# Performance work log

Measured on AMD Instinct MI355X. Metric: run time of the kernel, lower is better.

Reference implementation:

```python
import jax, jax.numpy as jnp
import numpy as np

DIM = 1024
HIDDEN = 4096
NNZ = 262144
X_SHAPE = (2, 256, DIM)


def setup_inputs() -> dict:
    key = jax.random.key(0)
    ks = jax.random.split(key, 13)
    return {
        "x": jax.random.normal(ks[0], X_SHAPE, dtype=jnp.float32),
        "up_row": jax.random.randint(ks[1], (NNZ,), 0, HIDDEN),
        "up_col": jax.random.randint(ks[2], (NNZ,), 0, DIM),
        "up_val": jax.random.normal(ks[3], (NNZ,), dtype=jnp.float32),
        "up_bias": jax.random.normal(ks[4], (HIDDEN,), dtype=jnp.float32),
        "gate_row": jax.random.randint(ks[5], (NNZ,), 0, HIDDEN),
        "gate_col": jax.random.randint(ks[6], (NNZ,), 0, DIM),
        "gate_val": jax.random.normal(ks[7], (NNZ,), dtype=jnp.float32),
        "gate_bias": jax.random.normal(ks[8], (HIDDEN,), dtype=jnp.float32),
        "down_row": jax.random.randint(ks[9], (NNZ,), 0, DIM),
        "down_col": jax.random.randint(ks[10], (NNZ,), 0, HIDDEN),
        "down_val": jax.random.normal(ks[11], (NNZ,), dtype=jnp.float32),
        "down_bias": jax.random.normal(ks[12], (DIM,), dtype=jnp.float32),
    }


def _sparse_linear(x2d, row, col, val, bias, out_features):
    # x2d: [T, in_features]; COO: row -> out_features, col -> in_features
    weighted = x2d[:, col] * val  # [T, nnz], same expanded form as torch gather*mul
    # scatter_add over rows == segment_sum over the nnz axis
    out = jax.ops.segment_sum(weighted.T, row, num_segments=out_features).T  # [T, out]
    return out + bias


def reference(x, up_row, up_col, up_val, up_bias,
              gate_row, gate_col, gate_val, gate_bias,
              down_row, down_col, down_val, down_bias):
    in_shape = x.shape
    x2d = x.reshape(-1, DIM)  # [T, dim]
    up = _sparse_linear(x2d, up_row, up_col, up_val, up_bias, HIDDEN)
    gate = _sparse_linear(x2d, gate_row, gate_col, gate_val, gate_bias, HIDDEN)
    hidden = jax.nn.silu(up) * gate  # [T, hidden]
    down = _sparse_linear(hidden, down_row, down_col, down_val, down_bias, DIM)
    return (x2d + down).reshape(in_shape)
```

## Files before the change

kernel.cpp:

```cpp
#include <hip/hip_runtime.h>
#include <hip/hip_bf16.h>
#include <stdint.h>


#define DIM_    1024
#define HIDDEN_ 4096
#define NNZ_    262144
#define TTOK_   512
#define PAD_    24

typedef __attribute__((ext_vector_type(8))) short short8;
typedef __attribute__((ext_vector_type(4))) float float4v;

__device__ inline unsigned short f2bf(float f) {
    union { float f; unsigned int u; } c; c.f = f;
    unsigned int u = c.u;
    unsigned int r = u + 0x7fffu + ((u >> 16) & 1u);
    return (unsigned short)(r >> 16);
}

__device__ inline void async16(const unsigned short* g, unsigned short* l) {
    __builtin_amdgcn_global_load_lds(
        (const __attribute__((address_space(1))) unsigned int*)g,
        (__attribute__((address_space(3))) unsigned int*)l, 16, 0, 0);
}

#define XC_ ((TTOK_ * DIM_) / 4)

__global__ __launch_bounds__(256) void bin_prep_kernel(
    const int* __restrict__ ur, const int* __restrict__ uc, const float* __restrict__ uv,
    const int* __restrict__ gr, const int* __restrict__ gc, const float* __restrict__ gv,
    const int* __restrict__ dr, const int* __restrict__ dc, const float* __restrict__ dv,
    const float* __restrict__ x, const float* __restrict__ down_bias,
    uint2* __restrict__ bands, int* __restrict__ cnt,
    unsigned short* __restrict__ xb, float* __restrict__ out) {
    const int b = blockIdx.x;
    const int t = threadIdx.x;
    if (b >= 768) {
        const unsigned int u0 = (b - 768) * 1024 + t * 4;
        #pragma unroll
        for (int q = 0; q < 4; ++q) {
            const unsigned int id = u0 + q;
            if (id < XC_) {
                float4 v = ((const float4*)x)[id];
                ushort4 o;
                o.x = f2bf(v.x); o.y = f2bf(v.y); o.z = f2bf(v.z); o.w = f2bf(v.w);
                ((ushort4*)xb)[id] = o;
            } else {
                const unsigned int i = id - XC_;
                float4 v = ((const float4*)x)[i];
                const int d = (i * 4) & (DIM_ - 1);
                const float4 bb = *(const float4*)(down_bias + d);
                float4 o;
                o.x = v.x + bb.x; o.y = v.y + bb.y; o.z = v.z + bb.z; o.w = v.w + bb.w;
                ((float4*)out)[i] = o;
            }
        }
        return;
    }
    __shared__ int lcount[256];
    const int mat = b >> 8;
    const int chunk = b & 255;
    const int*   rs = (mat == 0) ? ur : (mat == 1) ? gr : dr;
    const int*   cs = (mat == 0) ? uc : (mat == 1) ? gc : dc;
    const float* vs = (mat == 0) ? uv : (mat == 1) ? gv : dv;
    const int shift = (mat == 2) ? 2 : 4;
    const int rmask = (mat == 2) ? 3 : 15;
    lcount[t] = 0;
    __syncthreads();

    const int base = chunk * 1024 + t * 4;
    int4   r4 = *(const int4*)(rs + base);
    int4   c4 = *(const int4*)(cs + base);
    float4 v4 = *(const float4*)(vs + base);
    uint2* mbase = bands + mat * (256 * 256 * PAD_);
    int   rr[4] = {r4.x, r4.y, r4.z, r4.w};
    int   cc[4] = {c4.x, c4.y, c4.z, c4.w};
    float vv[4] = {v4.x, v4.y, v4.z, v4.w};
    #pragma unroll
    for (int j = 0; j < 4; ++j) {
        const int band = rr[j] >> shift;
        const int pos = atomicAdd(&lcount[band], 1);
        if (pos < PAD_) {
            uint2 e;
            e.x = ((unsigned int)(rr[j] & rmask) << 12) | (unsigned int)cc[j];
            e.y = __float_as_uint(vv[j]);
            mbase[(band * 256 + chunk) * PAD_ + pos] = e;
        }
    }
    __syncthreads();
    cnt[(mat * 256 + t) * 256 + chunk] = lcount[t];
}

__global__ __launch_bounds__(512) void build_kernel(
    const uint2* __restrict__ bands,
    const int* __restrict__ cnt,
    unsigned short* __restrict__ WUP,
    unsigned short* __restrict__ WGATE,
    unsigned short* __restrict__ WDOWN) {
    __shared__ float acc[16 * 1024];
    __shared__ int lcnt[256];
    const int b = blockIdx.x;
    const int t = threadIdx.x;
    const int mat = b >> 8;
    const int band = b & 255;
    unsigned int width;
    unsigned short* out;
    if (mat == 0)      { width = 1024; out = WUP + band * 16 * 1024; }
    else if (mat == 1) { width = 1024; out = WGATE + band * 16 * 1024; }
    else               { width = 4096; out = WDOWN + band * 4 * 4096; }

    for (int k = 0; k < 8; ++k)
        *(float4*)&acc[(k * 512 + t) * 4] = make_float4(0.f, 0.f, 0.f, 0.f);
    if (t < 256) lcnt[t] = cnt[(mat * 256 + band) * 256 + t];
    __syncthreads();

    const int chunk = t & 255;
    const int half = t >> 8;
    const uint2* seg = bands + (((mat * 256 + band) * 256) + chunk) * PAD_;
    const int c = lcnt[chunk];

    if (half == 0) {
        uint4 q[6];
        const uint4* sp = (const uint4*)seg;
        #pragma unroll
        for (int i = 0; i < 6; ++i) q[i] = sp[i];
        #pragma unroll
        for (int j = 0; j < 12; ++j) {
            const unsigned int ex = (j & 1) ? q[j >> 1].z : q[j >> 1].x;
            const unsigned int ey = (j & 1) ? q[j >> 1].w : q[j >> 1].y;
            if (j < c)
                atomicAdd(&acc[(ex >> 12) * width + (ex & 0xFFFu)],
                          __uint_as_float(ey));
        }
    } else {
        for (int j = 12; j < c && j < PAD_; ++j) {
            uint2 e = seg[j];
            atomicAdd(&acc[(e.x >> 12) * width + (e.x & 0xFFFu)],
                      __uint_as_float(e.y));
        }
    }
    __syncthreads();

    for (int k = 0; k < 8; ++k) {
        const int cc = (k * 512 + t) * 4;
        ushort4 o;
        o.x = f2bf(acc[cc]);     o.y = f2bf(acc[cc + 1]);
        o.z = f2bf(acc[cc + 2]); o.w = f2bf(acc[cc + 3]);
        *(ushort4*)(out + cc) = o;
    }
}

__global__ __launch_bounds__(256) void gemm_upgate_kernel(
    const unsigned short* __restrict__ xb,
    const unsigned short* __restrict__ wup,
    const unsigned short* __restrict__ wgate,
    const float* __restrict__ up_bias,
    const float* __restrict__ gate_bias,
    unsigned short* __restrict__ hid) {
    __shared__ unsigned short sA[2 * 64 * 32];
    __shared__ unsigned short sBu[2 * 64 * 32];
    __shared__ unsigned short sBg[2 * 64 * 32];
    const int t = threadIdx.x;
    const int n0 = blockIdx.x * 64;
    const int m0 = blockIdx.y * 64;
    const int w = t >> 6, l = t & 63;
    const int wm = (w >> 1) * 32, wn = (w & 1) * 32;
    const int lr = l & 15, lkq = (l >> 4);

    float4v au[2][2], ag[2][2];
    for (int im = 0; im < 2; ++im)
        for (int in = 0; in < 2; ++in) {
            au[im][in] = float4v{0.f, 0.f, 0.f, 0.f};
            ag[im][in] = float4v{0.f, 0.f, 0.f, 0.f};
        }

    const int srow = t >> 2, scol = (t & 3) * 8;
    const unsigned short* gA  = xb    + (m0 + srow) * DIM_ + scol;
    const unsigned short* gBu = wup   + (n0 + srow) * DIM_ + scol;
    const unsigned short* gBg = wgate + (n0 + srow) * DIM_ + scol;

    for (int k0 = 0; k0 < DIM_; k0 += 64) {
        async16(gA + k0,       &sA[t * 8]);
        async16(gA + k0 + 32,  &sA[2048 + t * 8]);
        async16(gBu + k0,      &sBu[t * 8]);
        async16(gBu + k0 + 32, &sBu[2048 + t * 8]);
        async16(gBg + k0,      &sBg[t * 8]);
        async16(gBg + k0 + 32, &sBg[2048 + t * 8]);
        __syncthreads();
        #pragma unroll
        for (int kk = 0; kk < 2; ++kk) {
            const int kb = kk * 2048 + lkq * 8;
            short8 a[2], bu[2], bg[2];
            for (int im = 0; im < 2; ++im)
                a[im] = *(const short8*)&sA[kb + (wm + im * 16 + lr) * 32];
            for (int in = 0; in < 2; ++in) {
                bu[in] = *(const short8*)&sBu[kb + (wn + in * 16 + lr) * 32];
                bg[in] = *(const short8*)&sBg[kb + (wn + in * 16 + lr) * 32];
            }
            for (int im = 0; im < 2; ++im)
                for (int in = 0; in < 2; ++in) {
                    au[im][in] = __builtin_amdgcn_mfma_f32_16x16x32_bf16(
                        a[im], bu[in], au[im][in], 0, 0, 0);
                    ag[im][in] = __builtin_amdgcn_mfma_f32_16x16x32_bf16(
                        a[im], bg[in], ag[im][in], 0, 0, 0);
                }
        }
        __syncthreads();
    }

    for (int im = 0; im < 2; ++im) {
        for (int in = 0; in < 2; ++in) {
            const int n = n0 + wn + in * 16 + lr;
            const float ub = up_bias[n], gb = gate_bias[n];
            for (int r = 0; r < 4; ++r) {
                const int m = m0 + wm + im * 16 + lkq * 4 + r;
                const float u = au[im][in][r] + ub;
                const float g = ag[im][in][r] + gb;
                const float h = (u / (1.f + __expf(-u))) * g;
                hid[m * HIDDEN_ + n] = f2bf(h);
            }
        }
    }
}

__global__ __launch_bounds__(256) void gemm_down_kernel(
    const unsigned short* __restrict__ hid,
    const unsigned short* __restrict__ wdown,
    float* __restrict__ out) {
    __shared__ unsigned short sA[2 * 64 * 32];
    __shared__ unsigned short sB[2 * 64 * 32];
    const int t = threadIdx.x;
    const int n0 = blockIdx.x * 64;
    const int m0 = blockIdx.y * 64;
    const int kb0 = blockIdx.z * 512;
    const int w = t >> 6, l = t & 63;
    const int wm = (w >> 1) * 32, wn = (w & 1) * 32;
    const int lr = l & 15, lkq = (l >> 4);

    float4v acc[2][2];
    for (int im = 0; im < 2; ++im)
        for (int in = 0; in < 2; ++in)
            acc[im][in] = float4v{0.f, 0.f, 0.f, 0.f};

    const int srow = t >> 2, scol = (t & 3) * 8;
    const unsigned short* gA = hid   + (m0 + srow) * HIDDEN_ + scol;
    const unsigned short* gB = wdown + (n0 + srow) * HIDDEN_ + scol;

    for (int k0 = kb0; k0 < kb0 + 512; k0 += 64) {
        async16(gA + k0,      &sA[t * 8]);
        async16(gA + k0 + 32, &sA[2048 + t * 8]);
        async16(gB + k0,      &sB[t * 8]);
        async16(gB + k0 + 32, &sB[2048 + t * 8]);
        __syncthreads();
        #pragma unroll
        for (int kk = 0; kk < 2; ++kk) {
            const int kb = kk * 2048 + lkq * 8;
            short8 a[2], b[2];
            for (int im = 0; im < 2; ++im)
                a[im] = *(const short8*)&sA[kb + (wm + im * 16 + lr) * 32];
            for (int in = 0; in < 2; ++in)
                b[in] = *(const short8*)&sB[kb + (wn + in * 16 + lr) * 32];
            for (int im = 0; im < 2; ++im)
                for (int in = 0; in < 2; ++in)
                    acc[im][in] = __builtin_amdgcn_mfma_f32_16x16x32_bf16(
                        a[im], b[in], acc[im][in], 0, 0, 0);
        }
        __syncthreads();
    }

    for (int im = 0; im < 2; ++im) {
        for (int in = 0; in < 2; ++in) {
            const int n = n0 + wn + in * 16 + lr;
            for (int r = 0; r < 4; ++r) {
                const int m = m0 + wm + im * 16 + lkq * 4 + r;
                atomicAdd(out + m * DIM_ + n, acc[im][in][r]);
            }
        }
    }
}

extern "C" void kernel_launch(void* const* d_in, const int* in_sizes, int n_in,
                              void* d_out, int out_size, void* d_ws, size_t ws_size,
                              hipStream_t stream) {
    const float* x         = (const float*)d_in[0];
    const int*   up_row    = (const int*)d_in[1];
    const int*   up_col    = (const int*)d_in[2];
    const float* up_val    = (const float*)d_in[3];
    const float* up_bias   = (const float*)d_in[4];
    const int*   gate_row  = (const int*)d_in[5];
    const int*   gate_col  = (const int*)d_in[6];
    const float* gate_val  = (const float*)d_in[7];
    const float* gate_bias = (const float*)d_in[8];
    const int*   down_row  = (const int*)d_in[9];
    const int*   down_col  = (const int*)d_in[10];
    const float* down_val  = (const float*)d_in[11];
    const float* down_bias = (const float*)d_in[12];
    float* out = (float*)d_out;

    unsigned char* ws = (unsigned char*)d_ws;
    unsigned short* WUP   = (unsigned short*)(ws);
    unsigned short* WGATE = (unsigned short*)(ws + (8u << 20));
    unsigned short* WDOWN = (unsigned short*)(ws + (16u << 20));
    unsigned short* XB    = (unsigned short*)(ws + (24u << 20));
    unsigned short* HID   = (unsigned short*)(ws + (25u << 20));
    uint2*          BANDS = (uint2*)(ws + (29u << 20));
    int*            CNT   = (int*)(ws + (66u << 20));

    bin_prep_kernel<<<1024, 256, 0, stream>>>(
        up_row, up_col, up_val, gate_row, gate_col, gate_val,
        down_row, down_col, down_val, x, down_bias, BANDS, CNT, XB, out);

    build_kernel<<<768, 512, 0, stream>>>(BANDS, CNT, WUP, WGATE, WDOWN);

    gemm_upgate_kernel<<<dim3(HIDDEN_ / 64, TTOK_ / 64), 256, 0, stream>>>(
        XB, WUP, WGATE, up_bias, gate_bias, HID);

    gemm_down_kernel<<<dim3(DIM_ / 64, TTOK_ / 64, 8), 256, 0, stream>>>(
        HID, WDOWN, out);
}
```

Baseline: 138.3 us.

## Overlap down-weight densification with up/gate GEMM in one fused launch

Splits the weight build kernel so only up/gate bands are densified first, then moves the down-projection band build into the up/gate GEMM launch. Every third block of the fused kernel scatters one down band into a 64KB shared accumulator and writes it as bf16, while the other blocks run the GEMM tiles. The aim is to hide the down build behind GEMM work and save a launch's tail. In exchange the fused kernel now reserves about 65KB of shared memory for every block, including the GEMM blocks, which may lower occupancy for the GEMM part.

```diff
diff --git a/kernel.cpp b/kernel.cpp
--- a/kernel.cpp
+++ b/kernel.cpp
@@ -92,23 +92,18 @@
     cnt[(mat * 256 + t) * 256 + chunk] = lcount[t];
 }
 
-__global__ __launch_bounds__(512) void build_kernel(
+__global__ __launch_bounds__(512) void build_upgate_kernel(
     const uint2* __restrict__ bands,
     const int* __restrict__ cnt,
     unsigned short* __restrict__ WUP,
-    unsigned short* __restrict__ WGATE,
-    unsigned short* __restrict__ WDOWN) {
+    unsigned short* __restrict__ WGATE) {
     __shared__ float acc[16 * 1024];
     __shared__ int lcnt[256];
     const int b = blockIdx.x;
     const int t = threadIdx.x;
     const int mat = b >> 8;
     const int band = b & 255;
-    unsigned int width;
-    unsigned short* out;
-    if (mat == 0)      { width = 1024; out = WUP + band * 16 * 1024; }
-    else if (mat == 1) { width = 1024; out = WGATE + band * 16 * 1024; }
-    else               { width = 4096; out = WDOWN + band * 4 * 4096; }
+    unsigned short* out = (mat == 0 ? WUP : WGATE) + band * 16 * 1024;
 
     for (int k = 0; k < 8; ++k)
         *(float4*)&acc[(k * 512 + t) * 4] = make_float4(0.f, 0.f, 0.f, 0.f);
@@ -130,13 +125,13 @@
             const unsigned int ex = (j & 1) ? q[j >> 1].z : q[j >> 1].x;
             const unsigned int ey = (j & 1) ? q[j >> 1].w : q[j >> 1].y;
             if (j < c)
-                atomicAdd(&acc[(ex >> 12) * width + (ex & 0xFFFu)],
+                atomicAdd(&acc[(ex >> 12) * 1024 + (ex & 0xFFFu)],
                           __uint_as_float(ey));
         }
     } else {
         for (int j = 12; j < c && j < PAD_; ++j) {
             uint2 e = seg[j];
-            atomicAdd(&acc[(e.x >> 12) * width + (e.x & 0xFFFu)],
+            atomicAdd(&acc[(e.x >> 12) * 1024 + (e.x & 0xFFFu)],
                       __uint_as_float(e.y));
         }
     }
@@ -151,19 +146,67 @@
     }
 }
 
-__global__ __launch_bounds__(256) void gemm_upgate_kernel(
+__global__ __launch_bounds__(256) void fused_upgate_builddown_kernel(
     const unsigned short* __restrict__ xb,
     const unsigned short* __restrict__ wup,
     const unsigned short* __restrict__ wgate,
     const float* __restrict__ up_bias,
     const float* __restrict__ gate_bias,
-    unsigned short* __restrict__ hid) {
-    __shared__ unsigned short sA[2 * 64 * 32];
-    __shared__ unsigned short sBu[2 * 64 * 32];
-    __shared__ unsigned short sBg[2 * 64 * 32];
+    unsigned short* __restrict__ hid,
+    const uint2* __restrict__ bands,
+    const int* __restrict__ cnt,
+    unsigned short* __restrict__ WDOWN) {
+    __shared__ __align__(16) unsigned char smem[66560];
+    const int b = blockIdx.x;
     const int t = threadIdx.x;
-    const int n0 = blockIdx.x * 64;
-    const int m0 = blockIdx.y * 64;
+
+    if (b % 3 == 2) {
+        float* acc = (float*)smem;
+        int* lcnt = (int*)(smem + 65536);
+        const int band = b / 3;
+        for (int k = 0; k < 16; ++k)
+            *(float4*)&acc[(k * 256 + t) * 4] = make_float4(0.f, 0.f, 0.f, 0.f);
+        lcnt[t] = cnt[(2 * 256 + band) * 256 + t];
+        __syncthreads();
+
+        const uint2* seg = bands + (((2 * 256 + band) * 256) + t) * PAD_;
+        const int c = lcnt[t];
+        uint4 q[6];
+        const uint4* sp = (const uint4*)seg;
+        #pragma unroll
+        for (int i = 0; i < 6; ++i) q[i] = sp[i];
+        #pragma unroll
+        for (int j = 0; j < 12; ++j) {
+            const unsigned int ex = (j & 1) ? q[j >> 1].z : q[j >> 1].x;
+            const unsigned int ey = (j & 1) ? q[j >> 1].w : q[j >> 1].y;
+            if (j < c)
+                atomicAdd(&acc[(ex >> 12) * 4096 + (ex & 0xFFFu)],
+                          __uint_as_float(ey));
+        }
+        for (int j = 12; j < c && j < PAD_; ++j) {
+            uint2 e = seg[j];
+            atomicAdd(&acc[(e.x >> 12) * 4096 + (e.x & 0xFFFu)],
+                      __uint_as_float(e.y));
+        }
+        __syncthreads();
+
+        unsigned short* out = WDOWN + band * 4 * 4096;
+        for (int k = 0; k < 16; ++k) {
+            const int cc = (k * 256 + t) * 4;
+            ushort4 o;
+            o.x = f2bf(acc[cc]);     o.y = f2bf(acc[cc + 1]);
+            o.z = f2bf(acc[cc + 2]); o.w = f2bf(acc[cc + 3]);
+            *(ushort4*)(out + cc) = o;
+        }
+        return;
+    }
+
+    unsigned short* sA  = (unsigned short*)smem;
+    unsigned short* sBu = sA + 4096;
+    unsigned short* sBg = sBu + 4096;
+    const int gidx = (b / 3) * 2 + (b % 3);
+    const int n0 = (gidx & 63) * 64;
+    const int m0 = (gidx >> 6) * 64;
     const int w = t >> 6, l = t & 63;
     const int wm = (w >> 1) * 32, wn = (w & 1) * 32;
     const int lr = l & 15, lkq = (l >> 4);
@@ -311,10 +354,10 @@
         up_row, up_col, up_val, gate_row, gate_col, gate_val,
         down_row, down_col, down_val, x, down_bias, BANDS, CNT, XB, out);
 
-    build_kernel<<<768, 512, 0, stream>>>(BANDS, CNT, WUP, WGATE, WDOWN);
-
-    gemm_upgate_kernel<<<dim3(HIDDEN_ / 64, TTOK_ / 64), 256, 0, stream>>>(
-        XB, WUP, WGATE, up_bias, gate_bias, HID);
+    build_upgate_kernel<<<512, 512, 0, stream>>>(BANDS, CNT, WUP, WGATE);
+
+    fused_upgate_builddown_kernel<<<768, 256, 0, stream>>>(
+        XB, WUP, WGATE, up_bias, gate_bias, HID, BANDS, CNT, WDOWN);
 
     gemm_down_kernel<<<dim3(DIM_ / 64, TTOK_ / 64, 8), 256, 0, stream>>>(
         HID, WDOWN, out);
```

Result: slower. 146.6 us (+6.0%).
